# Performance work log

Measured on AMD Instinct MI355X. Metric: run time of the kernel, lower is better.

## Reference

```python
import jax, jax.numpy as jnp
import numpy as np

HEADS = 8
DIM_HEAD = 32
SCALE = DIM_HEAD ** -0.5


def setup_inputs() -> dict:
    key = jax.random.key(0)
    k1, k2, k3 = jax.random.split(key, 3)
    dim = 256
    hidden = HEADS * DIM_HEAD  # 256
    x = jax.random.normal(k1, (2, dim, 16, 64, 64), dtype=jnp.float32)
    # 1x1 conv weights flattened to [out_ch, in_ch]
    w_qkv = jax.random.normal(k2, (hidden * 3, dim), dtype=jnp.float32) * (dim ** -0.5)
    w_out = jax.random.normal(k3, (dim, hidden), dtype=jnp.float32) * (hidden ** -0.5)
    b_out = jnp.zeros((dim,), dtype=jnp.float32)
    return {"x": x, "w_qkv": w_qkv, "w_out": w_out, "b_out": b_out}


def reference(x, w_qkv, w_out, b_out):
    b, c, f, h, w = x.shape
    n = h * w
    # 'b c f h w -> (b f) c (h w)'
    xf = jnp.transpose(x, (0, 2, 1, 3, 4)).reshape(b * f, c, n)
    # 1x1 conv projection: [3*hidden, c] @ [bf, c, n] -> [bf, 3*hidden, n]
    qkv = jnp.einsum('oc,bcn->bon', w_qkv, xf)
    hidden = w_qkv.shape[0] // 3
    q, k, v = jnp.split(qkv, 3, axis=1)
    # 'b (h d) n -> b h d n'
    def heads(t):
        return t.reshape(b * f, HEADS, hidden // HEADS, n)
    q, k, v = heads(q), heads(k), heads(v)
    q = jax.nn.softmax(q, axis=-2) * SCALE   # softmax over feature dim d
    k = jax.nn.softmax(k, axis=-1)           # softmax over spatial dim n
    # context: [bf, H, d, e]
    context = jnp.einsum('bhdn,bhen->bhde', k, v)
    out = jnp.einsum('bhde,bhdn->bhen', context, q)  # [bf, H, e, n]
    out = out.reshape(b * f, hidden, n)
    out = jnp.einsum('oc,bcn->bon', w_out, out) + b_out[None, :, None]
    # '(b f) c (h w) -> b c f h w'
    out = out.reshape(b, f, c, h, w).transpose(0, 2, 1, 3, 4)
    return out
```

## Files before the change

kernel.cpp:

```cpp
#include <hip/hip_runtime.h>
#include <math.h>

#define BB    2
#define CC    256
#define FF    16
#define NN    4096
#define FN    (FF*NN)
#define BF    32
#define HEADS 8
#define DH    32
#define HID   256
#define NS    8
#define TN1   64
#define TN3   64
#define SCALEF 0.17677669529663687f

#define WQHI_O  0
#define WQLO_O  65536
#define WKVHI_O 131072
#define WKVLO_O 262144
#define MHI_O   393216
#define MLO_O   (393216 + BF*256*256)
#define USH_ELEMS (393216 + 2*BF*256*256)

typedef __attribute__((ext_vector_type(8))) short bf16x8;
typedef __attribute__((ext_vector_type(8))) unsigned short u16x8;
typedef __attribute__((ext_vector_type(4))) unsigned short u16x4;
typedef __attribute__((ext_vector_type(4))) float f32x4;

#define MFMA16(a, b, c) __builtin_amdgcn_mfma_f32_16x16x32_bf16((a), (b), (c), 0, 0, 0)

__device__ __forceinline__ void bar_lgkm() {
    asm volatile("s_waitcnt lgkmcnt(0)" ::: "memory");
    __builtin_amdgcn_s_barrier();
    asm volatile("" ::: "memory");
}

__device__ inline unsigned short f2bf(float f) {
    unsigned int u = __float_as_uint(f);
    unsigned int r = (u + 0x7fffu + ((u >> 16) & 1u)) >> 16;
    return (unsigned short)r;
}
__device__ inline float bf2f(unsigned short h) {
    return __uint_as_float(((unsigned int)h) << 16);
}

__global__ __launch_bounds__(256) void k0_prep(const float* __restrict__ wqkv,
                                               unsigned short* __restrict__ wqfhi,
                                               unsigned short* __restrict__ wqflo,
                                               unsigned short* __restrict__ wkvfhi,
                                               unsigned short* __restrict__ wkvflo) {
    int idx = blockIdx.x * 256 + threadIdx.x;
    int o = idx >> 8;
    int c = idx & 255;
    float v = wqkv[idx];
    unsigned short hv = f2bf(v);
    unsigned short lv = f2bf(v - bf2f(hv));
    int kc = c >> 5, g = (c >> 3) & 3, i = c & 7;
    if (o < 256) {
        int w = o >> 5, rf = (o >> 4) & 1, m = o & 15;
        int fi = w * 8192 + rf * 4096 + kc * 512 + g * 128 + m * 8 + i;
        wqfhi[fi] = hv;
        wqflo[fi] = lv;
    } else {
        int r = o - 256;
        int w = r >> 6, cg = (r >> 4) & 3, m = r & 15;
        int fi = w * 16384 + cg * 4096 + kc * 512 + g * 128 + m * 8 + i;
        wkvfhi[fi] = hv;
        wkvflo[fi] = lv;
    }
}

__global__ __launch_bounds__(512, 2) void k1_mfma(const float* __restrict__ x,
                                                  const unsigned short* __restrict__ wkvfhi,
                                                  const unsigned short* __restrict__ wkvflo,
                                                  float* __restrict__ partC,
                                                  float* __restrict__ partz) {
    const int ns = blockIdx.x;
    const int bf = blockIdx.y;
    const int b = bf >> 4, f = bf & 15;
    const float* xbase = x + (size_t)b * (CC * FN) + (size_t)f * NN;
    const int t = threadIdx.x;
    const int w = t >> 6;
    const int l = t & 63;
    const int g = l >> 4, m = l & 15;

    const int strip = NN / NS;
    const int ntiles = strip / TN1;
    const int nbase = ns * strip;

    __shared__ __align__(16) char LDS[147456];
    char* X0 = LDS;
    char* X1 = LDS + 32768;
    char* PV0 = LDS + 65536 + w * 10240;
    char* PV1 = LDS + 65536 + w * 10240 + 5120;

    f32x4 ctx[2][2];
#pragma unroll
    for (int df = 0; df < 2; ++df)
#pragma unroll
        for (int ef = 0; ef < 2; ++ef) ctx[df][ef] = (f32x4)0.f;
    float zacc[2] = {0.f, 0.f};

    const int kbase = (w >> 1) * 16384 + (w & 1) * 8192 + l * 8;
    const int vbase = (4 + (w >> 1)) * 16384 + (w & 1) * 8192 + l * 8;
    const unsigned short* bkh = wkvfhi + kbase;
    const unsigned short* bkl = wkvflo + kbase;
    const unsigned short* bvh = wkvfhi + vbase;
    const unsigned short* bvl = wkvflo + vbase;

    const int nl = l;
    const int c0 = w * 32;

    float v[32];
#pragma unroll
    for (int i = 0; i < 32; ++i)
        v[i] = __builtin_nontemporal_load(&xbase[(size_t)(c0 + i) * FN + nbase + nl]);

#pragma unroll
    for (int qq = 0; qq < 4; ++qq) {
        u16x8 vh, vl;
#pragma unroll
        for (int i = 0; i < 8; ++i) {
            float fv = v[qq * 8 + i];
            unsigned short hv = f2bf(fv);
            vh[i] = hv;
            vl[i] = f2bf(fv - bf2f(hv));
        }
        int off = (nl * 512 + (c0 + qq * 8) * 2) ^ ((nl & 31) << 4);
        *(u16x8*)(X0 + off) = vh;
        *(u16x8*)(X1 + off) = vl;
    }
    if (ntiles > 1) {
#pragma unroll
        for (int i = 0; i < 32; ++i)
            v[i] = __builtin_nontemporal_load(&xbase[(size_t)(c0 + i) * FN + nbase + TN1 + nl]);
    }
    bar_lgkm();

    for (int tile = 0; tile < ntiles; ++tile) {
        f32x4 acc[4][4];
#pragma unroll
        for (int rf = 0; rf < 4; ++rf)
#pragma unroll
            for (int cg = 0; cg < 4; ++cg) acc[rf][cg] = (f32x4)0.f;

#pragma unroll 2
        for (int kc = 0; kc < 8; ++kc) {
            bf16x8 ah[4], al[4];
#pragma unroll
            for (int rf = 0; rf < 4; ++rf) {
                int n = 16 * rf + m;
                int off = (n * 512 + (32 * kc + 8 * g) * 2) ^ ((n & 31) << 4);
                ah[rf] = *(const bf16x8*)(X0 + off);
                al[rf] = *(const bf16x8*)(X1 + off);
            }
            bf16x8 bh[4], bl[4];
            bh[0] = *(const bf16x8*)(bkh + kc * 512);
            bl[0] = *(const bf16x8*)(bkl + kc * 512);
            bh[1] = *(const bf16x8*)(bkh + 4096 + kc * 512);
            bl[1] = *(const bf16x8*)(bkl + 4096 + kc * 512);
            bh[2] = *(const bf16x8*)(bvh + kc * 512);
            bl[2] = *(const bf16x8*)(bvl + kc * 512);
            bh[3] = *(const bf16x8*)(bvh + 4096 + kc * 512);
            bl[3] = *(const bf16x8*)(bvl + 4096 + kc * 512);
#pragma unroll
            for (int rf = 0; rf < 4; ++rf)
#pragma unroll
                for (int cg = 0; cg < 4; ++cg) {
                    acc[rf][cg] = MFMA16(ah[rf], bh[cg], acc[rf][cg]);
                    acc[rf][cg] = MFMA16(ah[rf], bl[cg], acc[rf][cg]);
                    acc[rf][cg] = MFMA16(al[rf], bh[cg], acc[rf][cg]);
                }
        }
        bar_lgkm();

#pragma unroll
        for (int cg = 0; cg < 2; ++cg) {
            float s = 0.f;
#pragma unroll
            for (int rf = 0; rf < 4; ++rf)
#pragma unroll
                for (int r = 0; r < 4; ++r) {
                    float e = __expf(acc[rf][cg][r]);
                    acc[rf][cg][r] = e;
                    s += e;
                }
            s += __shfl_xor(s, 16);
            s += __shfl_xor(s, 32);
            zacc[cg] += s;
        }

#pragma unroll
        for (int ks = 0; ks < 2; ++ks) {
#pragma unroll
            for (int rfh = 0; rfh < 2; ++rfh) {
                int rf = 2 * ks + rfh;
#pragma unroll
                for (int cg = 0; cg < 4; ++cg) {
                    int row = 16 * cg + m;
                    u16x4 vh4, vl4;
#pragma unroll
                    for (int r = 0; r < 4; ++r) {
                        float fv = acc[rf][cg][r];
                        unsigned short hv = f2bf(fv);
                        vh4[r] = hv;
                        vl4[r] = f2bf(fv - bf2f(hv));
                    }
                    int off = row * 80 + 32 * rfh + 8 * g;
                    *(u16x4*)(PV0 + off) = vh4;
                    *(u16x4*)(PV1 + off) = vl4;
                }
            }
            bf16x8 ph[2], pl[2], vh_[2], vl_[2];
#pragma unroll
            for (int df = 0; df < 2; ++df) {
                int off = (16 * df + m) * 80 + 16 * g;
                ph[df] = *(const bf16x8*)(PV0 + off);
                pl[df] = *(const bf16x8*)(PV1 + off);
            }
#pragma unroll
            for (int ef = 0; ef < 2; ++ef) {
                int off = (32 + 16 * ef + m) * 80 + 16 * g;
                vh_[ef] = *(const bf16x8*)(PV0 + off);
                vl_[ef] = *(const bf16x8*)(PV1 + off);
            }
#pragma unroll
            for (int df = 0; df < 2; ++df)
#pragma unroll
                for (int ef = 0; ef < 2; ++ef) {
                    ctx[df][ef] = MFMA16(ph[df], vh_[ef], ctx[df][ef]);
                    ctx[df][ef] = MFMA16(ph[df], vl_[ef], ctx[df][ef]);
                    ctx[df][ef] = MFMA16(pl[df], vh_[ef], ctx[df][ef]);
                }
        }

        if (tile + 1 < ntiles) {
#pragma unroll
            for (int qq = 0; qq < 4; ++qq) {
                u16x8 vh, vl;
#pragma unroll
                for (int i = 0; i < 8; ++i) {
                    float fv = v[qq * 8 + i];
                    unsigned short hv = f2bf(fv);
                    vh[i] = hv;
                    vl[i] = f2bf(fv - bf2f(hv));
                }
                int off = (nl * 512 + (c0 + qq * 8) * 2) ^ ((nl & 31) << 4);
                *(u16x8*)(X0 + off) = vh;
                *(u16x8*)(X1 + off) = vl;
            }
            if (tile + 2 < ntiles) {
                int n0n = nbase + (tile + 2) * TN1;
#pragma unroll
                for (int i = 0; i < 32; ++i)
                    v[i] = __builtin_nontemporal_load(&xbase[(size_t)(c0 + i) * FN + n0n + nl]);
            }
            bar_lgkm();
        }
    }

    if (g == 0) {
#pragma unroll
        for (int cg = 0; cg < 2; ++cg)
            partz[(size_t)(bf * NS + ns) * 256 + 32 * w + 16 * cg + m] = zacc[cg];
    }
#pragma unroll
    for (int df = 0; df < 2; ++df)
#pragma unroll
        for (int ef = 0; ef < 2; ++ef)
#pragma unroll
            for (int r = 0; r < 4; ++r) {
                int row = 32 * w + 16 * df + 4 * g + r;
                int col = 16 * ef + m;
                partC[((size_t)(bf * NS + ns) * 256 + row) * 32 + col] = ctx[df][ef][r];
            }
}

__global__ __launch_bounds__(256) void k2_M(const float* __restrict__ partC,
                                            const float* __restrict__ partz,
                                            const float* __restrict__ wout,
                                            unsigned short* __restrict__ Mhi,
                                            unsigned short* __restrict__ Mlo,
                                            int nsplit) {
    const int bf = blockIdx.x;
    const int t = threadIdx.x;
    const int h = t >> 5;
    const int kc = t >> 5, g = (t >> 3) & 3, ii = t & 7;

    float z = 0.f;
    for (int ns2 = 0; ns2 < nsplit; ++ns2) z += partz[(size_t)(bf * nsplit + ns2) * 256 + t];
    float inv = SCALEF / z;
    float ctx[32];
#pragma unroll
    for (int e = 0; e < 32; ++e) ctx[e] = 0.f;
    for (int ns2 = 0; ns2 < nsplit; ++ns2) {
        const float* pc = partC + ((size_t)(bf * nsplit + ns2) * 256 + t) * 32;
#pragma unroll
        for (int e = 0; e < 32; ++e) ctx[e] += pc[e];
    }
#pragma unroll
    for (int e = 0; e < 32; ++e) ctx[e] *= inv;

    __shared__ float wos[8][256];
    for (int ob = 0; ob < 256; ob += 8) {
        __syncthreads();
#pragma unroll
        for (int i = 0; i < 8; ++i) wos[i][t] = wout[(ob + i) * 256 + t];
        __syncthreads();
#pragma unroll
        for (int oo = 0; oo < 8; ++oo) {
            int o = ob + oo;
            float mv = 0.f;
#pragma unroll
            for (int e = 0; e < 32; ++e) mv += wos[oo][32 * h + e] * ctx[e];
            unsigned short hv = f2bf(mv);
            unsigned short lv = f2bf(mv - bf2f(hv));
            int wq = o >> 5, rf = (o >> 4) & 1, mm = o & 15;
            size_t fi = (size_t)bf * 65536 + wq * 8192 + rf * 4096 + kc * 512
                      + g * 128 + mm * 8 + ii;
            Mhi[fi] = hv;
            Mlo[fi] = lv;
        }
    }
}

__global__ __launch_bounds__(512, 4) void k3_mfma(const float* __restrict__ x,
                                                  const unsigned short* __restrict__ wqfhi,
                                                  const unsigned short* __restrict__ wqflo,
                                                  const unsigned short* __restrict__ mfhi,
                                                  const unsigned short* __restrict__ mflo,
                                                  const float* __restrict__ bout,
                                                  float* __restrict__ out) {
    const int tile = blockIdx.x;
    const int bf = blockIdx.y;
    const int b = bf >> 4, f = bf & 15;
    const size_t xoff = (size_t)b * (CC * FN) + (size_t)f * NN;
    const float* xg = x + xoff;
    float* og = out + xoff;
    const int n0 = tile * TN3;
    const int t = threadIdx.x;
    const int w = t >> 6;
    const int l = t & 63;
    const int g = l >> 4, m = l & 15;

    __shared__ unsigned short lds[2][64][256];
    char* L0 = (char*)&lds[0][0][0];
    char* L1 = (char*)&lds[1][0][0];

#pragma unroll
    for (int q = 0; q < 4; ++q) {
        int c0 = 32 * w + 8 * q;
        float v[8];
#pragma unroll
        for (int i = 0; i < 8; ++i)
            v[i] = __builtin_nontemporal_load(&xg[(size_t)(c0 + i) * FN + n0 + l]);
        u16x8 vh, vl;
#pragma unroll
        for (int i = 0; i < 8; ++i) {
            unsigned short hv = f2bf(v[i]);
            vh[i] = hv;
            vl[i] = f2bf(v[i] - bf2f(hv));
        }
        int off = (l * 512 + c0 * 2) ^ ((l & 31) << 4);
        *(u16x8*)(L0 + off) = vh;
        *(u16x8*)(L1 + off) = vl;
    }
    __syncthreads();

    const unsigned short* aqh = wqfhi + w * 8192 + l * 8;
    const unsigned short* aql = wqflo + w * 8192 + l * 8;

    f32x4 qacc[2][4];
#pragma unroll
    for (int rf = 0; rf < 2; ++rf)
#pragma unroll
        for (int cg = 0; cg < 4; ++cg) qacc[rf][cg] = (f32x4)0.f;

    for (int kc = 0; kc < 8; ++kc) {
        bf16x8 ah[2], al[2];
#pragma unroll
        for (int rf = 0; rf < 2; ++rf) {
            ah[rf] = *(const bf16x8*)(aqh + rf * 4096 + kc * 512);
            al[rf] = *(const bf16x8*)(aql + rf * 4096 + kc * 512);
        }
        bf16x8 bh[4], bl[4];
#pragma unroll
        for (int cg = 0; cg < 4; ++cg) {
            int n = 16 * cg + m;
            int off = (n * 512 + (32 * kc + 8 * g) * 2) ^ ((n & 31) << 4);
            bh[cg] = *(const bf16x8*)(L0 + off);
            bl[cg] = *(const bf16x8*)(L1 + off);
        }
#pragma unroll
        for (int rf = 0; rf < 2; ++rf)
#pragma unroll
            for (int cg = 0; cg < 4; ++cg) {
                qacc[rf][cg] = MFMA16(ah[rf], bh[cg], qacc[rf][cg]);
                qacc[rf][cg] = MFMA16(ah[rf], bl[cg], qacc[rf][cg]);
                qacc[rf][cg] = MFMA16(al[rf], bh[cg], qacc[rf][cg]);
            }
    }

    float zinv[4];
#pragma unroll
    for (int cg = 0; cg < 4; ++cg) {
        float s = 0.f;
#pragma unroll
        for (int rf = 0; rf < 2; ++rf)
#pragma unroll
            for (int r = 0; r < 4; ++r) {
                float e = __expf(qacc[rf][cg][r]);
                qacc[rf][cg][r] = e;
                s += e;
            }
        s += __shfl_xor(s, 16);
        s += __shfl_xor(s, 32);
        zinv[cg] = 1.f / s;
    }

    __syncthreads();

#pragma unroll
    for (int rf = 0; rf < 2; ++rf)
#pragma unroll
        for (int cg = 0; cg < 4; ++cg) {
            int n = 16 * cg + m;
            int hd0 = 32 * w + 16 * rf + 4 * g;
            u16x4 vh, vl;
#pragma unroll
            for (int r = 0; r < 4; ++r) {
                float qv = qacc[rf][cg][r] * zinv[cg];
                unsigned short hv = f2bf(qv);
                vh[r] = hv;
                vl[r] = f2bf(qv - bf2f(hv));
            }
            int off = (n * 512 + hd0 * 2) ^ ((n & 31) << 4);
            *(u16x4*)(L0 + off) = vh;
            *(u16x4*)(L1 + off) = vl;
        }
    __syncthreads();

    f32x4 oacc[2][4];
#pragma unroll
    for (int rf = 0; rf < 2; ++rf)
#pragma unroll
        for (int cg = 0; cg < 4; ++cg) oacc[rf][cg] = (f32x4)0.f;

    const unsigned short* Mh = mfhi + (size_t)bf * 65536 + w * 8192 + l * 8;
    const unsigned short* Ml = mflo + (size_t)bf * 65536 + w * 8192 + l * 8;
    for (int kc = 0; kc < 8; ++kc) {
        bf16x8 ah[2], al[2];
#pragma unroll
        for (int rf = 0; rf < 2; ++rf) {
            ah[rf] = *(const bf16x8*)(Mh + rf * 4096 + kc * 512);
            al[rf] = *(const bf16x8*)(Ml + rf * 4096 + kc * 512);
        }
        bf16x8 bh[4], bl[4];
#pragma unroll
        for (int cg = 0; cg < 4; ++cg) {
            int n = 16 * cg + m;
            int off = (n * 512 + (32 * kc + 8 * g) * 2) ^ ((n & 31) << 4);
            bh[cg] = *(const bf16x8*)(L0 + off);
            bl[cg] = *(const bf16x8*)(L1 + off);
        }
#pragma unroll
        for (int rf = 0; rf < 2; ++rf)
#pragma unroll
            for (int cg = 0; cg < 4; ++cg) {
                oacc[rf][cg] = MFMA16(ah[rf], bh[cg], oacc[rf][cg]);
                oacc[rf][cg] = MFMA16(ah[rf], bl[cg], oacc[rf][cg]);
                oacc[rf][cg] = MFMA16(al[rf], bh[cg], oacc[rf][cg]);
            }
    }

#pragma unroll
    for (int rf = 0; rf < 2; ++rf) {
        float bb[4];
#pragma unroll
        for (int r = 0; r < 4; ++r) bb[r] = bout[32 * w + 16 * rf + 4 * g + r];
#pragma unroll
        for (int cg = 0; cg < 4; ++cg) {
            int n = n0 + 16 * cg + m;
#pragma unroll
            for (int r = 0; r < 4; ++r) {
                int o = 32 * w + 16 * rf + 4 * g + r;
                __builtin_nontemporal_store(oacc[rf][cg][r] + bb[r], &og[(size_t)o * FN + n]);
            }
        }
    }
}

extern "C" void kernel_launch(void* const* d_in, const int* in_sizes, int n_in,
                              void* d_out, int out_size, void* d_ws, size_t ws_size,
                              hipStream_t stream) {
    const float* x    = (const float*)d_in[0];
    const float* wqkv = (const float*)d_in[1];
    const float* wout = (const float*)d_in[2];
    const float* bout = (const float*)d_in[3];
    float* out = (float*)d_out;
    float* ws  = (float*)d_ws;

    size_t partc_elems = (size_t)BF * NS * 256 * 32;
    size_t partz_elems = (size_t)BF * NS * 256;
    float* partC = ws;
    float* partz = ws + partc_elems;
    unsigned short* U = (unsigned short*)(ws + partc_elems + partz_elems);
    unsigned short* wqfhi  = U + WQHI_O;
    unsigned short* wqflo  = U + WQLO_O;
    unsigned short* wkvfhi = U + WKVHI_O;
    unsigned short* wkvflo = U + WKVLO_O;
    unsigned short* Mfhi   = U + MHI_O;
    unsigned short* Mflo   = U + MLO_O;

    k0_prep<<<768, 256, 0, stream>>>(wqkv, wqfhi, wqflo, wkvfhi, wkvflo);
    k1_mfma<<<dim3(NS, BF), 512, 0, stream>>>(x, wkvfhi, wkvflo, partC, partz);
    k2_M<<<BF, 256, 0, stream>>>(partC, partz, wout, Mfhi, Mflo, NS);
    k3_mfma<<<dim3(NN / TN3, BF), 512, 0, stream>>>(x, wqfhi, wqflo, Mfhi, Mflo, bout, out);
}
```

Measured before the change: 311.9 us.

## Split k2_M across heads and stage context in shared memory

```diff
diff --git a/kernel.cpp b/kernel.cpp
--- a/kernel.cpp
+++ b/kernel.cpp
@@ -1,4 +1,5 @@
 #include <hip/hip_runtime.h>
+#include <hip/hip_bf16.h>
 #include <math.h>
 
 #define BB    2
@@ -37,9 +38,9 @@
 }
 
 __device__ inline unsigned short f2bf(float f) {
-    unsigned int u = __float_as_uint(f);
-    unsigned int r = (u + 0x7fffu + ((u >> 16) & 1u)) >> 16;
-    return (unsigned short)r;
+    union { __hip_bfloat16 h; unsigned short u; } cv;
+    cv.h = __float2bfloat16(f);
+    return cv.u;
 }
 __device__ inline float bf2f(unsigned short h) {
     return __uint_as_float(((unsigned int)h) << 16);
@@ -284,44 +285,57 @@
                                             unsigned short* __restrict__ Mlo,
                                             int nsplit) {
     const int bf = blockIdx.x;
-    const int t = threadIdx.x;
-    const int h = t >> 5;
-    const int kc = t >> 5, g = (t >> 3) & 3, ii = t & 7;
-
-    float z = 0.f;
-    for (int ns2 = 0; ns2 < nsplit; ++ns2) z += partz[(size_t)(bf * nsplit + ns2) * 256 + t];
-    float inv = SCALEF / z;
-    float ctx[32];
-#pragma unroll
-    for (int e = 0; e < 32; ++e) ctx[e] = 0.f;
-    for (int ns2 = 0; ns2 < nsplit; ++ns2) {
-        const float* pc = partC + ((size_t)(bf * nsplit + ns2) * 256 + t) * 32;
-#pragma unroll
-        for (int e = 0; e < 32; ++e) ctx[e] += pc[e];
-    }
-#pragma unroll
-    for (int e = 0; e < 32; ++e) ctx[e] *= inv;
-
-    __shared__ float wos[8][256];
-    for (int ob = 0; ob < 256; ob += 8) {
+    const int h  = blockIdx.y;
+    const int t  = threadIdx.x;
+
+    __shared__ float ctxs[32][33];
+    __shared__ float zs[32];
+
+    if (t < 32) {
+        float z = 0.f;
+        for (int ns2 = 0; ns2 < nsplit; ++ns2)
+            z += partz[(size_t)(bf * nsplit + ns2) * 256 + 32 * h + t];
+        zs[t] = SCALEF / z;
+    }
+    {
+        const int d = t & 31, eg = t >> 5;
+        float4 c = make_float4(0.f, 0.f, 0.f, 0.f);
+        for (int ns2 = 0; ns2 < nsplit; ++ns2) {
+            const float4 p = *(const float4*)&partC[
+                ((size_t)(bf * nsplit + ns2) * 256 + 32 * h + d) * 32 + 4 * eg];
+            c.x += p.x; c.y += p.y; c.z += p.z; c.w += p.w;
+        }
         __syncthreads();
-#pragma unroll
-        for (int i = 0; i < 8; ++i) wos[i][t] = wout[(ob + i) * 256 + t];
-        __syncthreads();
-#pragma unroll
-        for (int oo = 0; oo < 8; ++oo) {
-            int o = ob + oo;
-            float mv = 0.f;
-#pragma unroll
-            for (int e = 0; e < 32; ++e) mv += wos[oo][32 * h + e] * ctx[e];
-            unsigned short hv = f2bf(mv);
-            unsigned short lv = f2bf(mv - bf2f(hv));
-            int wq = o >> 5, rf = (o >> 4) & 1, mm = o & 15;
-            size_t fi = (size_t)bf * 65536 + wq * 8192 + rf * 4096 + kc * 512
-                      + g * 128 + mm * 8 + ii;
-            Mhi[fi] = hv;
-            Mlo[fi] = lv;
-        }
+        float zi = zs[d];
+        ctxs[d][4 * eg + 0] = c.x * zi;
+        ctxs[d][4 * eg + 1] = c.y * zi;
+        ctxs[d][4 * eg + 2] = c.z * zi;
+        ctxs[d][4 * eg + 3] = c.w * zi;
+    }
+    __syncthreads();
+
+    const int o = t;
+    float wo[32];
+#pragma unroll
+    for (int j = 0; j < 8; ++j) {
+        float4 w4 = *(const float4*)&wout[o * 256 + 32 * h + 4 * j];
+        wo[4 * j + 0] = w4.x;
+        wo[4 * j + 1] = w4.y;
+        wo[4 * j + 2] = w4.z;
+        wo[4 * j + 3] = w4.w;
+    }
+    const int wq = o >> 5, rf = (o >> 4) & 1, mm = o & 15;
+    const size_t fbase = (size_t)bf * 65536 + wq * 8192 + rf * 4096 + h * 512 + mm * 8;
+#pragma unroll
+    for (int d = 0; d < 32; ++d) {
+        float mv = 0.f;
+#pragma unroll
+        for (int e = 0; e < 32; ++e) mv += wo[e] * ctxs[d][e];
+        unsigned short hv = f2bf(mv);
+        unsigned short lv = f2bf(mv - bf2f(hv));
+        size_t fi = fbase + (size_t)(d >> 3) * 128 + (d & 7);
+        Mhi[fi] = hv;
+        Mlo[fi] = lv;
     }
 }
 
@@ -515,6 +529,6 @@
 
     k0_prep<<<768, 256, 0, stream>>>(wqkv, wqfhi, wqflo, wkvfhi, wkvflo);
     k1_mfma<<<dim3(NS, BF), 512, 0, stream>>>(x, wkvfhi, wkvflo, partC, partz);
-    k2_M<<<BF, 256, 0, stream>>>(partC, partz, wout, Mfhi, Mflo, NS);
+    k2_M<<<dim3(BF, HEADS), 256, 0, stream>>>(partC, partz, wout, Mfhi, Mflo, NS);
     k3_mfma<<<dim3(NN / TN3, BF), 512, 0, stream>>>(x, wqfhi, wqflo, Mfhi, Mflo, bout, out);
 }
```

Result: faster. 258.7 us (-17.1%).
